# Kernel optimization log

Measured on AMD Instinct MI355X. Metric: run time of the kernel, lower is better.

Reference implementation:

```python
import jax, jax.numpy as jnp
import numpy as np

D_MODEL = 1024
N_HEADS = 16
HEAD_DIM = D_MODEL // N_HEADS  # 64
WINDOW = 128
LOCAL_BLOCK = 256
LATENT_TOKENS = 64
LATENT_D = 256
LATENT_HEADS = 4
LATENT_HD = LATENT_D // LATENT_HEADS  # 64
NEG = -1e9


def setup_inputs() -> dict:
    key = jax.random.key(0)
    ks = jax.random.split(key, 14)
    B, S = 2, 4096
    s = 0.02
    f32 = jnp.float32
    return {
        "x": jax.random.normal(ks[0], (B, S, D_MODEL), f32),
        "qkv_w": jax.random.normal(ks[1], (D_MODEL, 3 * D_MODEL), f32) * s,
        "qkv_b": jnp.zeros((3 * D_MODEL,), f32),
        "rq_w": jax.random.normal(ks[2], (D_MODEL, LATENT_D), f32) * s,
        "rq_b": jnp.zeros((LATENT_D,), f32),
        "rkv_w": jax.random.normal(ks[3], (D_MODEL, 2 * LATENT_D), f32) * s,
        "rkv_b": jnp.zeros((2 * LATENT_D,), f32),
        "rout_w": jax.random.normal(ks[4], (LATENT_D, D_MODEL), f32) * s,
        "rout_b": jnp.zeros((D_MODEL,), f32),
        "out_w": jax.random.normal(ks[5], (D_MODEL, D_MODEL), f32) * s,
        "out_b": jnp.zeros((D_MODEL,), f32),
        "gl_w": jax.random.normal(ks[6], (HEAD_DIM, 1), f32) * s,
        "gr_w": jax.random.normal(ks[7], (HEAD_DIM, 1), f32) * s,
    }


def _local_attention(q, k, v):
    # q,k,v: [B,H,S,hd]. Blockwise causal local attention: query i attends to
    # keys at distance d with 0 < d <= WINDOW (strictly past, self excluded).
    B, H, S, hd = q.shape
    bs = min(S, max(WINDOW, LOCAL_BLOCK))
    nb = S // bs  # S chosen divisible by bs
    w = WINDOW
    L = bs + w - 1  # key span per query block
    k_pad = jnp.pad(k, ((0, 0), (0, 0), (w - 1, 0), (0, 0)))
    v_pad = jnp.pad(v, ((0, 0), (0, 0), (w - 1, 0), (0, 0)))
    starts = jnp.arange(nb) * bs
    idx = starts[:, None] + jnp.arange(L)[None, :]  # [nb,L] into padded axis
    kb = k_pad[:, :, idx]  # [B,H,nb,L,hd]
    vb = v_pad[:, :, idx]
    qb = q.reshape(B, H, nb, bs, hd)
    q_pos = starts[:, None] + jnp.arange(bs)[None, :]            # [nb,bs]
    k_gpos = starts[:, None] + jnp.arange(L)[None, :] - (w - 1)   # [nb,L]
    dist = q_pos[:, :, None] - k_gpos[:, None, :]                 # [nb,bs,L]
    allowed = (dist > 0) & (dist <= w) & (k_gpos[:, None, :] >= 0)
    scale = 1.0 / np.sqrt(hd)
    scores = jnp.einsum('bhnqd,bhnkd->bhnqk', qb, kb) * scale
    scores = jnp.where(allowed, scores, NEG)
    attn = jax.nn.softmax(scores, axis=-1)
    # query 0 has no valid keys (self excluded) -> output 0 for that row
    attn = jnp.where(allowed.any(-1)[None, None, :, :, None], attn, 0.0)
    out = jnp.einsum('bhnqk,bhnkd->bhnqd', attn, vb)
    return out.reshape(B, H, S, hd)


def reference(x, qkv_w, qkv_b, rq_w, rq_b, rkv_w, rkv_b, rout_w, rout_b,
              out_w, out_b, gl_w, gr_w):
    B, S, D = x.shape
    # ---- local branch ----
    qkv = x @ qkv_w + qkv_b  # [B,S,3D]
    q, k, v = jnp.split(qkv, 3, axis=-1)
    def heads(t):
        return t.reshape(B, S, N_HEADS, HEAD_DIM).transpose(0, 2, 1, 3)
    local = _local_attention(heads(q), heads(k), heads(v))  # [B,H,S,hd]
    # ---- pooled latents ----
    chunk = -(-S // min(LATENT_TOKENS, S))  # ceil; S divisible here
    nlat = S // chunk
    pooled = x.reshape(B, nlat, chunk, D).mean(axis=2)  # [B,L,D]
    chunk_ids = jnp.arange(S) // chunk                   # [S]
    # ---- latent cross-attention ----
    rq = (x @ rq_w + rq_b).reshape(B, S, LATENT_HEADS, LATENT_HD).transpose(0, 2, 1, 3)
    rkv = pooled @ rkv_w + rkv_b
    rk, rv = jnp.split(rkv, 2, axis=-1)
    rk = rk.reshape(B, nlat, LATENT_HEADS, LATENT_HD).transpose(0, 2, 1, 3)
    rv = rv.reshape(B, nlat, LATENT_HEADS, LATENT_HD).transpose(0, 2, 1, 3)
    lscale = 1.0 / np.sqrt(LATENT_HD)
    lscores = jnp.einsum('bhsd,bhld->bhsl', rq, rk) * lscale  # [B,Hl,S,L]
    lat_allowed = jnp.arange(nlat)[None, :] < chunk_ids[:, None]  # strictly past chunks
    lscores = jnp.where(lat_allowed[None, None], lscores, NEG)
    lattn = jax.nn.softmax(lscores, axis=-1)
    lattn = jnp.where(lat_allowed.any(-1)[None, None, :, None], lattn, 0.0)
    lat_out = jnp.einsum('bhsl,bhld->bhsd', lattn, rv)  # [B,Hl,S,hdl]
    lat_out = lat_out.transpose(0, 2, 1, 3).reshape(B, S, LATENT_D)
    remote = (lat_out @ rout_w + rout_b)                 # [B,S,D]
    remote_h = remote.reshape(B, S, N_HEADS, HEAD_DIM).transpose(0, 2, 1, 3)
    # ---- learned per-head gate mixing local/remote ----
    gate = jax.nn.sigmoid(local @ gl_w + remote_h @ gr_w)  # [B,H,S,1]
    mixed = gate * local + (1.0 - gate) * remote_h
    mixed = mixed.transpose(0, 2, 1, 3).reshape(B, S, D)
    return mixed @ out_w + out_b
```

## Files before the change

### kernel.cpp

```cpp
#include <hip/hip_runtime.h>

typedef __bf16 bf16;
typedef bf16 bf16x4 __attribute__((ext_vector_type(4)));
typedef bf16 bf16x8 __attribute__((ext_vector_type(8)));
typedef float f32x4 __attribute__((ext_vector_type(4)));

#define B_ 2
#define S_ 4096
#define D_ 1024
#define QSTR 3328

__device__ __forceinline__ void gload_lds16(const void* g, void* l) {
  __builtin_amdgcn_global_load_lds((const __attribute__((address_space(1))) void*)g,
                                   (__attribute__((address_space(3))) void*)l, 16, 0, 0);
}

__device__ __forceinline__ void transpose_block(
    const float* __restrict__ in, bf16* __restrict__ out, int K, int N,
    int bx, int by, float (*tile)[33], int tx, int ty)
{
  const int nb = bx * 32, kb = by * 32;
#pragma unroll
  for (int j = 0; j < 4; j++)
    tile[ty + j * 8][tx] = in[(size_t)(kb + ty + j * 8) * N + nb + tx];
  __syncthreads();
#pragma unroll
  for (int j = 0; j < 4; j++)
    out[(size_t)(nb + ty + j * 8) * K + kb + tx] = (bf16)tile[tx][ty + j * 8];
}

__global__ __launch_bounds__(256) void prep_kernel(
    const float* __restrict__ qkv_w, const float* __restrict__ rq_w,
    const float* __restrict__ rkv_w, const float* __restrict__ rout_w,
    const float* __restrict__ out_w, const float* __restrict__ x,
    const float* __restrict__ qkv_b, const float* __restrict__ rq_b,
    bf16* __restrict__ qkvr_wt, bf16* __restrict__ rkv_wt,
    bf16* __restrict__ rout_wt, bf16* __restrict__ out_wt,
    bf16* __restrict__ xb, float* __restrict__ qkvr_b)
{
  __shared__ float tile[32][33];
  const int t = threadIdx.x;
  const int tx = t & 31, ty = t >> 5;
  int bid = blockIdx.x;
  if (bid < 3072) {
    transpose_block(qkv_w, qkvr_wt, 1024, 3072, bid % 96, bid / 96, tile, tx, ty);
    return;
  }
  bid -= 3072;
  if (bid < 256) {
    transpose_block(rq_w, qkvr_wt + (size_t)3072 * 1024, 1024, 256, bid % 8, bid / 8, tile, tx, ty);
    return;
  }
  bid -= 256;
  if (bid < 512) {
    transpose_block(rkv_w, rkv_wt, 1024, 512, bid % 16, bid / 16, tile, tx, ty);
    return;
  }
  bid -= 512;
  if (bid < 256) {
    transpose_block(rout_w, rout_wt, 256, 1024, bid % 32, bid / 32, tile, tx, ty);
    return;
  }
  bid -= 256;
  if (bid < 1024) {
    transpose_block(out_w, out_wt, 1024, 1024, bid % 32, bid / 32, tile, tx, ty);
    return;
  }
  bid -= 1024;
  if (bid < 2048) {
    const int n4 = B_ * S_ * 1024 / 4;
    for (int i = bid * 256 + t; i < n4; i += 2048 * 256) {
      const float4 v = ((const float4*)x)[i];
      bf16x4 o = {(bf16)v.x, (bf16)v.y, (bf16)v.z, (bf16)v.w};
      *(bf16x4*)&xb[i * 4] = o;
    }
    return;
  }
  {
    for (int i = t; i < 3072; i += 256) qkvr_b[i] = qkv_b[i];
    if (t < 256) qkvr_b[3072 + t] = rq_b[t];
  }
}

template <typename OutT>
__global__ __launch_bounds__(256) void gemm_bias_kernel(
    const bf16* __restrict__ A, const bf16* __restrict__ Bt,
    const float* __restrict__ bias, OutT* __restrict__ C,
    int M, int N, int K)
{
  __shared__ __align__(16) bf16 Al[128 * 32];
  __shared__ __align__(16) bf16 Bl[128 * 32];
  const int m0 = blockIdx.x * 128;
  const int n0 = blockIdx.y * 128;
  const int t = threadIdx.x;
  const int lane = t & 63;
  const int wave = t >> 6;
  const int wr = (wave >> 1) * 64;
  const int wc = (wave & 1) * 64;
  const int r16 = lane & 15;
  const int kg = lane >> 4;

  f32x4 acc[4][4];
#pragma unroll
  for (int i = 0; i < 4; i++)
#pragma unroll
    for (int j = 0; j < 4; j++) {
      f32x4 z = {0.f, 0.f, 0.f, 0.f};
      acc[i][j] = z;
    }

  for (int k0 = 0; k0 < K; k0 += 32) {
    __syncthreads();
#pragma unroll
    for (int i = 0; i < 2; i++) {
      const int o = i * 4096 + wave * 1024 + lane * 16;
      const int r = o >> 6;
      const int cb = o & 63;
      gload_lds16((const char*)(A + (size_t)(m0 + r) * K + k0) + cb,
                  (char*)Al + i * 4096 + wave * 1024);
      gload_lds16((const char*)(Bt + (size_t)(n0 + r) * K + k0) + cb,
                  (char*)Bl + i * 4096 + wave * 1024);
    }
    __syncthreads();
    bf16x8 a[4], b[4];
#pragma unroll
    for (int i = 0; i < 4; i++)
      a[i] = *(const bf16x8*)&Al[(wr + i * 16 + r16) * 32 + kg * 8];
#pragma unroll
    for (int i = 0; i < 4; i++)
      b[i] = *(const bf16x8*)&Bl[(wc + i * 16 + r16) * 32 + kg * 8];
#pragma unroll
    for (int i = 0; i < 4; i++)
#pragma unroll
      for (int j = 0; j < 4; j++)
        acc[i][j] = __builtin_amdgcn_mfma_f32_16x16x32_bf16(a[i], b[j], acc[i][j], 0, 0, 0);
  }

  float bs[4];
#pragma unroll
  for (int j = 0; j < 4; j++) bs[j] = bias[n0 + wc + j * 16 + r16];
#pragma unroll
  for (int i = 0; i < 4; i++)
#pragma unroll
    for (int j = 0; j < 4; j++)
#pragma unroll
      for (int r = 0; r < 4; r++) {
        const int row = m0 + wr + i * 16 + kg * 4 + r;
        const int col = n0 + wc + j * 16 + r16;
        C[(size_t)row * N + col] = (OutT)(acc[i][j][r] + bs[j]);
      }
}

template <typename OutT>
__global__ __launch_bounds__(512, 1) void gemm8_kernel(
    const bf16* __restrict__ A, const bf16* __restrict__ Bt,
    const float* __restrict__ bias, OutT* __restrict__ C,
    int M, int N, int K)
{
  __shared__ __align__(16) bf16 Al[2][256 * 64];
  __shared__ __align__(16) bf16 Bl[2][256 * 64];

  const int nbx = gridDim.x;
  const int nwg = nbx * gridDim.y;
  int bid = blockIdx.y * nbx + blockIdx.x;
  bid = (bid & 7) * (nwg >> 3) + (bid >> 3);
  const int m0 = (bid % nbx) * 256;
  const int n0 = (bid / nbx) * 256;

  const int t = threadIdx.x;
  const int lane = t & 63;
  const int w = t >> 6;
  const int wm = w >> 2;
  const int wn = w & 3;
  const int l15 = lane & 15;
  const int kg = lane >> 4;

  const int srow = t >> 3;
  const int schunk = (t & 7) ^ (srow & 7);
  const bf16* Aaddr = A + (size_t)(m0 + srow) * K + schunk * 8;
  const bf16* Baddr = Bt + (size_t)(n0 + srow) * K + schunk * 8;

  const int NT = K >> 6;
  const int NITER = NT >> 1;

  const int arow = wm * 128 + l15;
  const int brow = wn * 64 + l15;
  const int c0 = (kg ^ (l15 & 7)) * 16;
  const int c1 = ((4 + kg) ^ (l15 & 7)) * 16;

  f32x4 acc[8][4];
#pragma unroll
  for (int i = 0; i < 8; i++)
#pragma unroll
    for (int j = 0; j < 4; j++) { f32x4 z = {0, 0, 0, 0}; acc[i][j] = z; }

#define STG_A(buf, q, kt) gload_lds16(Aaddr + (size_t)(q) * 64 * K + (kt) * 64, \
                                      (char*)&Al[buf][0] + (q) * 8192 + w * 1024)
#define STG_B(buf, q, kt) gload_lds16(Baddr + (size_t)(q) * 64 * K + (kt) * 64, \
                                      (char*)&Bl[buf][0] + (q) * 8192 + w * 1024)
#define RD_A(buf, aq) \
  _Pragma("unroll") for (int ii = 0; ii < 4; ii++) { \
    const char* p_ = (const char*)&Al[buf][0] + (size_t)(arow + (aq) * 64 + ii * 16) * 128; \
    af[ii][0] = *(const bf16x8*)(p_ + c0); \
    af[ii][1] = *(const bf16x8*)(p_ + c1); }
#define RD_B(buf) \
  _Pragma("unroll") for (int jj = 0; jj < 4; jj++) { \
    const char* p_ = (const char*)&Bl[buf][0] + (size_t)(brow + jj * 16) * 128; \
    bfr[jj][0] = *(const bf16x8*)(p_ + c0); \
    bfr[jj][1] = *(const bf16x8*)(p_ + c1); }
#define MM(iofs, j0) \
  _Pragma("unroll") for (int ii = 0; ii < 4; ii++) \
  _Pragma("unroll") for (int jj = (j0); jj < (j0) + 2; jj++) { \
    acc[(iofs) + ii][jj] = __builtin_amdgcn_mfma_f32_16x16x32_bf16(af[ii][0], bfr[jj][0], acc[(iofs) + ii][jj], 0, 0, 0); \
    acc[(iofs) + ii][jj] = __builtin_amdgcn_mfma_f32_16x16x32_bf16(af[ii][1], bfr[jj][1], acc[(iofs) + ii][jj], 0, 0, 0); }
#define BARX __builtin_amdgcn_s_barrier()
#define LGKMD asm volatile("s_waitcnt lgkmcnt(0)" ::: "memory")
#define PRI1 __builtin_amdgcn_s_setprio(1)
#define PRI0 __builtin_amdgcn_s_setprio(0)

#pragma unroll
  for (int q = 0; q < 4; q++) { STG_B(0, q, 0); }
#pragma unroll
  for (int q = 0; q < 4; q++) { STG_A(0, q, 0); }
#pragma unroll
  for (int q = 0; q < 4; q++) { STG_B(1, q, 1); }
#pragma unroll
  for (int q = 0; q < 4; q++) { STG_A(1, q, 1); }
  asm volatile("s_waitcnt vmcnt(8)" ::: "memory");
  BARX;

  bf16x8 af[4][2], bfr[4][2];

  for (int it = 0; it < NITER; it++) {
    const int kt0 = 2 * it;
    const bool st = (it + 1) < NITER;

    RD_A(0, 0); RD_B(0);
    PRI1; MM(0, 0); PRI0; LGKMD; BARX;
    if (st) { STG_B(0, 0, kt0 + 2); STG_B(0, 1, kt0 + 2); }
    PRI1; MM(0, 2); PRI0; BARX;
    RD_A(0, 1);
    if (st) { STG_B(0, 2, kt0 + 2); STG_B(0, 3, kt0 + 2); }
    PRI1; MM(4, 0); PRI0; LGKMD; BARX;
    if (st) { STG_A(0, 0, kt0 + 2); STG_A(0, 2, kt0 + 2); }
    PRI1; MM(4, 2); PRI0;
    asm volatile("s_waitcnt vmcnt(6)" ::: "memory");
    BARX;

    RD_A(1, 0); RD_B(1);
    if (st) { STG_A(0, 1, kt0 + 2); STG_A(0, 3, kt0 + 2); }
    PRI1; MM(0, 0); PRI0; LGKMD; BARX;
    if (st) { STG_B(1, 0, kt0 + 3); STG_B(1, 1, kt0 + 3); }
    PRI1; MM(0, 2); PRI0; BARX;
    RD_A(1, 1);
    if (st) { STG_B(1, 2, kt0 + 3); STG_B(1, 3, kt0 + 3); }
    PRI1; MM(4, 0); PRI0; LGKMD; BARX;
    if (st) { STG_A(1, 0, kt0 + 3); STG_A(1, 1, kt0 + 3);
              STG_A(1, 2, kt0 + 3); STG_A(1, 3, kt0 + 3); }
    PRI1; MM(4, 2); PRI0;
    asm volatile("s_waitcnt vmcnt(8)" ::: "memory");
    BARX;
  }

#undef STG_A
#undef STG_B
#undef RD_A
#undef RD_B
#undef MM
#undef BARX
#undef LGKMD
#undef PRI1
#undef PRI0

  float bs[4];
#pragma unroll
  for (int j = 0; j < 4; j++) bs[j] = bias[n0 + wn * 64 + j * 16 + l15];
#pragma unroll
  for (int i = 0; i < 8; i++)
#pragma unroll
    for (int j = 0; j < 4; j++)
#pragma unroll
      for (int rr = 0; rr < 4; rr++) {
        const int row = m0 + wm * 128 + i * 16 + kg * 4 + rr;
        const int col = n0 + wn * 64 + j * 16 + l15;
        C[(size_t)row * N + col] = (OutT)(acc[i][j][rr] + bs[j]);
      }
}

__global__ __launch_bounds__(256) void pool_rkv_kernel(
    const bf16* __restrict__ xb, const bf16* __restrict__ rkv_wt,
    const float* __restrict__ rkv_b, bf16* __restrict__ rkvb)
{
  __shared__ float prow[1024];
  const int blk = blockIdx.x;
  const int b = blk >> 6, lt = blk & 63;
  const int t = threadIdx.x;

  const bf16* px = xb + ((size_t)b * S_ + lt * 64) * 1024 + t * 4;
  float s0 = 0.f, s1 = 0.f, s2 = 0.f, s3 = 0.f;
#pragma unroll
  for (int c = 0; c < 64; c++) {
    bf16x4 v = *(const bf16x4*)(px + (size_t)c * 1024);
    s0 += (float)v[0]; s1 += (float)v[1]; s2 += (float)v[2]; s3 += (float)v[3];
  }
  prow[t * 4 + 0] = s0 * 0.015625f;
  prow[t * 4 + 1] = s1 * 0.015625f;
  prow[t * 4 + 2] = s2 * 0.015625f;
  prow[t * 4 + 3] = s3 * 0.015625f;
  __syncthreads();

  const int n = blockIdx.y * 256 + t;
  const bf16* wcol = rkv_wt + (size_t)n * 1024;
  float s = rkv_b[n];
#pragma unroll 4
  for (int k = 0; k < 1024; k += 8) {
    bf16x8 wv = *(const bf16x8*)(wcol + k);
#pragma unroll
    for (int j = 0; j < 8; j++) s += prow[k + j] * (float)wv[j];
  }
  rkvb[(size_t)blk * 512 + n] = (bf16)s;
}

__global__ __launch_bounds__(256) void latent_attn_kernel(
    const bf16* __restrict__ qkvrb, const bf16* __restrict__ rkvb,
    bf16* __restrict__ latout)
{
  __shared__ float rq_s[256];
  __shared__ float attn_s[4][64];
  const int blk = blockIdx.x;
  const int b = blk >> 12, s = blk & 4095;
  const int t = threadIdx.x;
  const int h = t >> 6, l = t & 63;
  const int cid = s >> 6;
  rq_s[t] = (float)qkvrb[((size_t)b * S_ + s) * QSTR + 3072 + t];
  __syncthreads();
  float val = -1e30f;
  if (l < cid) {
    const bf16* kr = rkvb + (size_t)(b * 64 + l) * 512 + h * 64;
    float sum = 0.f;
#pragma unroll
    for (int c = 0; c < 8; c++) {
      bf16x8 kv = *(const bf16x8*)(kr + c * 8);
#pragma unroll
      for (int j = 0; j < 8; j++) sum += rq_s[h * 64 + c * 8 + j] * (float)kv[j];
    }
    val = sum * 0.125f;
  }
  float mx = val;
#pragma unroll
  for (int off = 32; off; off >>= 1) mx = fmaxf(mx, __shfl_xor(mx, off));
  const float p = (l < cid) ? __expf(val - mx) : 0.f;
  float sm = p;
#pragma unroll
  for (int off = 32; off; off >>= 1) sm += __shfl_xor(sm, off);
  attn_s[h][l] = (sm > 0.f) ? p / sm : 0.f;
  __syncthreads();
  float o = 0.f;
  const bf16* vb = rkvb + (size_t)b * 64 * 512 + 256 + h * 64 + l;
  for (int lat = 0; lat < cid; lat++) o += attn_s[h][lat] * (float)vb[(size_t)lat * 512];
  latout[((size_t)b * S_ + s) * 256 + h * 64 + l] = (bf16)o;
}

__global__ __launch_bounds__(256, 4) void local_attn_gate(
    const bf16* __restrict__ qkv, const bf16* __restrict__ remote,
    const float* __restrict__ glw, const float* __restrict__ grw,
    bf16* __restrict__ mixedb)
{
  __shared__ __align__(16) bf16 Kl[128 * 72];
  __shared__ __align__(16) bf16 Vt[64 * 136];
  __shared__ __align__(16) bf16 Pl[4][16 * 136];

  const int q0 = blockIdx.x * 128;
  const int h  = blockIdx.y;
  const int b  = blockIdx.z;
  const int t  = threadIdx.x;
  const int w  = t >> 6;
  const int l  = t & 63;
  const int g  = l >> 4;
  const int l15 = l & 15;

  const bf16* qbase = qkv + (size_t)b * S_ * QSTR + h * 64;
  const bf16* kbase = qbase + 1024;
  const bf16* vbase = qbase + 2048;

  bf16* PlW = &Pl[w][0];

  const int vrow = (t >> 3) * 4;
  const int vdh  = (t & 7) * 8;

  bf16x8 qf[2][2];
#pragma unroll
  for (int sl = 0; sl < 2; sl++) {
    const int j = sl ? 7 - w : w;
#pragma unroll
    for (int db = 0; db < 2; db++)
      qf[sl][db] = *(const bf16x8*)(qbase + (size_t)(q0 + j * 16 + l15) * QSTR + db * 32 + g * 8);
  }

  float m_[2][4], l_[2][4];
  f32x4 accO[2][4];
#pragma unroll
  for (int sl = 0; sl < 2; sl++) {
#pragma unroll
    for (int r = 0; r < 4; r++) { m_[sl][r] = -1e30f; l_[sl][r] = 0.f; }
#pragma unroll
    for (int dt = 0; dt < 4; dt++) { f32x4 z = {0,0,0,0}; accO[sl][dt] = z; }
  }

  const int tstart = (q0 == 0) ? 1 : 0;

  for (int tile = tstart; tile < 2; tile++) {
    const int base = q0 - 128 + tile * 128;
    bf16x8 kreg[4], vreg[4];
#pragma unroll
    for (int i = 0; i < 4; i++) {
      const int c = i * 256 + t;
      const int kk = c >> 3, dc = c & 7;
      kreg[i] = *(const bf16x8*)(kbase + (size_t)(base + kk) * QSTR + dc * 8);
    }
#pragma unroll
    for (int i = 0; i < 4; i++)
      vreg[i] = *(const bf16x8*)(vbase + (size_t)(base + vrow + i) * QSTR + vdh);

    __syncthreads();
#pragma unroll
    for (int i = 0; i < 4; i++) {
      const int c = i * 256 + t;
      const int kk = c >> 3, dc = c & 7;
      *(bf16x8*)&Kl[kk * 72 + dc * 8] = kreg[i];
    }
#pragma unroll
    for (int j = 0; j < 8; j++) {
      bf16x4 wv = {vreg[0][j], vreg[1][j], vreg[2][j], vreg[3][j]};
      *(bf16x4*)&Vt[(vdh + j) * 136 + vrow] = wv;
    }
    __syncthreads();

#pragma unroll
    for (int sl = 0; sl < 2; sl++) {
      const int j = sl ? 7 - w : w;
      const int lo = (tile == 0) ? (j & ~1) : 0;
      const int hi = (tile == 0) ? 8 : ((j & ~1) + 2);

      f32x4 s[8];
      __builtin_amdgcn_s_setprio(1);
#pragma unroll
      for (int kk = 0; kk < 8; kk++) {
        if (kk < lo || kk >= hi) continue;
        f32x4 z = {0,0,0,0};
        s[kk] = z;
        const bf16x8 kf0 = *(const bf16x8*)&Kl[(kk * 16 + l15) * 72 + g * 8];
        const bf16x8 kf1 = *(const bf16x8*)&Kl[(kk * 16 + l15) * 72 + 32 + g * 8];
        s[kk] = __builtin_amdgcn_mfma_f32_16x16x32_bf16(qf[sl][0], kf0, s[kk], 0, 0, 0);
        s[kk] = __builtin_amdgcn_mfma_f32_16x16x32_bf16(qf[sl][1], kf1, s[kk], 0, 0, 0);
      }
      __builtin_amdgcn_s_setprio(0);
#pragma unroll
      for (int kk = 0; kk < 8; kk++) {
        if (kk < lo || kk >= hi) continue;
        const int kr = kk * 16 + l15;
#pragma unroll
        for (int r = 0; r < 4; r++) {
          const int qr = j * 16 + g * 4 + r;
          const bool ok = (tile == 0) ? (kr >= qr) : (kr < qr);
          s[kk][r] = ok ? s[kk][r] * 0.125f : -1e9f;
        }
      }
      float corr[4];
#pragma unroll
      for (int r = 0; r < 4; r++) {
        float v = -1e30f;
#pragma unroll
        for (int kk = 0; kk < 8; kk++) { if (kk < lo || kk >= hi) continue; v = fmaxf(v, s[kk][r]); }
        v = fmaxf(v, __shfl_xor(v, 1));
        v = fmaxf(v, __shfl_xor(v, 2));
        v = fmaxf(v, __shfl_xor(v, 4));
        v = fmaxf(v, __shfl_xor(v, 8));
        const float mn = fmaxf(m_[sl][r], v);
        corr[r] = __expf(m_[sl][r] - mn);
        m_[sl][r] = mn;
      }
      float rs[4] = {0.f, 0.f, 0.f, 0.f};
#pragma unroll
      for (int kk = 0; kk < 8; kk++) {
        if (kk < lo || kk >= hi) continue;
#pragma unroll
        for (int r = 0; r < 4; r++) {
          const float sv = s[kk][r];
          const float p = (sv > -5e8f) ? __expf(sv - m_[sl][r]) : 0.f;
          rs[r] += p;
          PlW[(g * 4 + r) * 136 + kk * 16 + l15] = (bf16)p;
        }
      }
#pragma unroll
      for (int r = 0; r < 4; r++) {
        float v = rs[r];
        v += __shfl_xor(v, 1); v += __shfl_xor(v, 2);
        v += __shfl_xor(v, 4); v += __shfl_xor(v, 8);
        l_[sl][r] = l_[sl][r] * corr[r] + v;
#pragma unroll
        for (int dt = 0; dt < 4; dt++) accO[sl][dt][r] *= corr[r];
      }
      const int clo = (tile == 0) ? (j >> 1) : 0;
      const int chi = (tile == 0) ? 4 : ((j >> 1) + 1);
      __builtin_amdgcn_s_setprio(1);
#pragma unroll
      for (int kc = 0; kc < 4; kc++) {
        if (kc < clo || kc >= chi) continue;
        const bf16x8 pa = *(const bf16x8*)&PlW[l15 * 136 + kc * 32 + g * 8];
#pragma unroll
        for (int dt = 0; dt < 4; dt++) {
          const bf16x8 vf = *(const bf16x8*)&Vt[(dt * 16 + l15) * 136 + kc * 32 + g * 8];
          accO[sl][dt] = __builtin_amdgcn_mfma_f32_16x16x32_bf16(pa, vf, accO[sl][dt], 0, 0, 0);
        }
      }
      __builtin_amdgcn_s_setprio(0);
    }
  }

  float glv[4], grv[4];
#pragma unroll
  for (int dt = 0; dt < 4; dt++) {
    glv[dt] = glw[dt * 16 + l15];
    grv[dt] = grw[dt * 16 + l15];
  }
  bf16* outp = mixedb + ((size_t)b * S_ + q0) * 1024 + h * 64;
  const bf16* rbase = remote + ((size_t)b * S_ + q0) * 1024 + h * 64;
#pragma unroll
  for (int sl = 0; sl < 2; sl++) {
    const int j = sl ? 7 - w : w;
#pragma unroll
    for (int r = 0; r < 4; r++) {
      const int row = j * 16 + g * 4 + r;
      const float inv = (l_[sl][r] > 0.f) ? 1.f / l_[sl][r] : 0.f;
      float lv[4], rv[4];
      float part = 0.f;
#pragma unroll
      for (int dt = 0; dt < 4; dt++) {
        lv[dt] = accO[sl][dt][r] * inv;
        rv[dt] = (float)rbase[(size_t)row * 1024 + dt * 16 + l15];
        part += lv[dt] * glv[dt] + rv[dt] * grv[dt];
      }
      part += __shfl_xor(part, 1);
      part += __shfl_xor(part, 2);
      part += __shfl_xor(part, 4);
      part += __shfl_xor(part, 8);
      const float gg = 1.f / (1.f + __expf(-part));
#pragma unroll
      for (int dt = 0; dt < 4; dt++)
        outp[(size_t)row * 1024 + dt * 16 + l15] = (bf16)(gg * lv[dt] + (1.f - gg) * rv[dt]);
    }
  }
}

extern "C" void kernel_launch(void* const* d_in, const int* in_sizes, int n_in,
                              void* d_out, int out_size, void* d_ws, size_t ws_size,
                              hipStream_t stream)
{
  const float* x      = (const float*)d_in[0];
  const float* qkv_w  = (const float*)d_in[1];
  const float* qkv_b  = (const float*)d_in[2];
  const float* rq_w   = (const float*)d_in[3];
  const float* rq_b   = (const float*)d_in[4];
  const float* rkv_w  = (const float*)d_in[5];
  const float* rkv_b  = (const float*)d_in[6];
  const float* rout_w = (const float*)d_in[7];
  const float* rout_b = (const float*)d_in[8];
  const float* out_w  = (const float*)d_in[9];
  const float* out_b  = (const float*)d_in[10];
  const float* gl_w   = (const float*)d_in[11];
  const float* gr_w   = (const float*)d_in[12];

  char* w = (char*)d_ws;
  bf16* qkvr_wt = (bf16*)w; w += (size_t)QSTR * 1024 * 2;
  bf16* rkv_wt  = (bf16*)w; w += (size_t)512 * 1024 * 2;
  bf16* rout_wt = (bf16*)w; w += (size_t)1024 * 256 * 2;
  bf16* out_wt  = (bf16*)w; w += (size_t)1024 * 1024 * 2;
  float* qkvr_b = (float*)w; w += (size_t)QSTR * 4;
  bf16* xb      = (bf16*)w; w += (size_t)B_ * S_ * 1024 * 2;
  bf16* qkvrb   = (bf16*)w; w += (size_t)B_ * S_ * QSTR * 2;
  bf16* rkvb    = (bf16*)w; w += (size_t)B_ * 64 * 512 * 2;
  bf16* latout  = (bf16*)w; w += (size_t)B_ * S_ * 256 * 2;
  bf16* remote  = (bf16*)w; w += (size_t)B_ * S_ * 1024 * 2;
  bf16* mixedb  = (bf16*)w; w += (size_t)B_ * S_ * 1024 * 2;

  prep_kernel<<<dim3(7169), 256, 0, stream>>>(qkv_w, rq_w, rkv_w, rout_w, out_w, x,
                                              qkv_b, rq_b,
                                              qkvr_wt, rkv_wt, rout_wt, out_wt, xb, qkvr_b);

  gemm8_kernel<bf16><<<dim3(32, 13), 512, 0, stream>>>(xb, qkvr_wt, qkvr_b, qkvrb, B_ * S_, QSTR, 1024);
  pool_rkv_kernel<<<dim3(128, 2), 256, 0, stream>>>(xb, rkv_wt, rkv_b, rkvb);
  latent_attn_kernel<<<dim3(B_ * S_), 256, 0, stream>>>(qkvrb, rkvb, latout);
  gemm_bias_kernel<bf16><<<dim3(64, 8), 256, 0, stream>>>(latout, rout_wt, rout_b, remote, B_ * S_, 1024, 256);
  local_attn_gate<<<dim3(S_ / 128, 16, B_), 256, 0, stream>>>(qkvrb, remote, gl_w, gr_w, mixedb);
  gemm_bias_kernel<float><<<dim3(64, 8), 256, 0, stream>>>(mixedb, out_wt, out_b, (float*)d_out, B_ * S_, 1024, 1024);
}
```

Before: 216.0 us.

## Restructure GEMM mainloop into per-tile pipeline with staggered A/B prefetch

Replaces the two-tile unrolled mainloop with a single-k-tile loop that alternates LDS buffers. A is prefetched one tile ahead into the other buffer, and B is prefetched two tiles ahead into the buffer being consumed, once its reads are done. B fragment reads are split into two halves, so MFMA phases interleave more finely with LDS reads and global-to-LDS loads. The intent is better overlap of memory traffic with MFMA work. The cost is more barriers per tile and careful vmcnt and lgkmcnt accounting, which could create hazards or stalls.

```diff
diff --git a/kernel.cpp b/kernel.cpp
--- a/kernel.cpp
+++ b/kernel.cpp
@@ -181,7 +181,6 @@
   const bf16* Baddr = Bt + (size_t)(n0 + srow) * K + schunk * 8;
 
   const int NT = K >> 6;
-  const int NITER = NT >> 1;
 
   const int arow = wm * 128 + l15;
   const int brow = wn * 64 + l15;
@@ -194,17 +193,28 @@
 #pragma unroll
     for (int j = 0; j < 4; j++) { f32x4 z = {0, 0, 0, 0}; acc[i][j] = z; }
 
-#define STG_A(buf, q, kt) gload_lds16(Aaddr + (size_t)(q) * 64 * K + (kt) * 64, \
-                                      (char*)&Al[buf][0] + (q) * 8192 + w * 1024)
-#define STG_B(buf, q, kt) gload_lds16(Baddr + (size_t)(q) * 64 * K + (kt) * 64, \
-                                      (char*)&Bl[buf][0] + (q) * 8192 + w * 1024)
+#define STG_A(buf, half, kt) do { \
+  gload_lds16(Aaddr + (size_t)((half) * 128) * K + (kt) * 64, \
+              (char*)&Al[buf][0] + (half) * 16384 + w * 1024); \
+  gload_lds16(Aaddr + (size_t)((half) * 128 + 64) * K + (kt) * 64, \
+              (char*)&Al[buf][0] + (half) * 16384 + 8192 + w * 1024); } while (0)
+#define STG_B(buf, half, kt) do { \
+  gload_lds16(Baddr + (size_t)((half) * 128) * K + (kt) * 64, \
+              (char*)&Bl[buf][0] + (half) * 16384 + w * 1024); \
+  gload_lds16(Baddr + (size_t)((half) * 128 + 64) * K + (kt) * 64, \
+              (char*)&Bl[buf][0] + (half) * 16384 + 8192 + w * 1024); } while (0)
 #define RD_A(buf, aq) \
   _Pragma("unroll") for (int ii = 0; ii < 4; ii++) { \
     const char* p_ = (const char*)&Al[buf][0] + (size_t)(arow + (aq) * 64 + ii * 16) * 128; \
     af[ii][0] = *(const bf16x8*)(p_ + c0); \
     af[ii][1] = *(const bf16x8*)(p_ + c1); }
-#define RD_B(buf) \
-  _Pragma("unroll") for (int jj = 0; jj < 4; jj++) { \
+#define RD_B01(buf) \
+  _Pragma("unroll") for (int jj = 0; jj < 2; jj++) { \
+    const char* p_ = (const char*)&Bl[buf][0] + (size_t)(brow + jj * 16) * 128; \
+    bfr[jj][0] = *(const bf16x8*)(p_ + c0); \
+    bfr[jj][1] = *(const bf16x8*)(p_ + c1); }
+#define RD_B23(buf) \
+  _Pragma("unroll") for (int jj = 2; jj < 4; jj++) { \
     const char* p_ = (const char*)&Bl[buf][0] + (size_t)(brow + jj * 16) * 128; \
     bfr[jj][0] = *(const bf16x8*)(p_ + c0); \
     bfr[jj][1] = *(const bf16x8*)(p_ + c1); }
@@ -214,61 +224,54 @@
     acc[(iofs) + ii][jj] = __builtin_amdgcn_mfma_f32_16x16x32_bf16(af[ii][0], bfr[jj][0], acc[(iofs) + ii][jj], 0, 0, 0); \
     acc[(iofs) + ii][jj] = __builtin_amdgcn_mfma_f32_16x16x32_bf16(af[ii][1], bfr[jj][1], acc[(iofs) + ii][jj], 0, 0, 0); }
 #define BARX __builtin_amdgcn_s_barrier()
-#define LGKMD asm volatile("s_waitcnt lgkmcnt(0)" ::: "memory")
+#define LGKM0 asm volatile("s_waitcnt lgkmcnt(0)" ::: "memory")
 #define PRI1 __builtin_amdgcn_s_setprio(1)
 #define PRI0 __builtin_amdgcn_s_setprio(0)
 
-#pragma unroll
-  for (int q = 0; q < 4; q++) { STG_B(0, q, 0); }
-#pragma unroll
-  for (int q = 0; q < 4; q++) { STG_A(0, q, 0); }
-#pragma unroll
-  for (int q = 0; q < 4; q++) { STG_B(1, q, 1); }
-#pragma unroll
-  for (int q = 0; q < 4; q++) { STG_A(1, q, 1); }
-  asm volatile("s_waitcnt vmcnt(8)" ::: "memory");
+  STG_B(0, 0, 0); STG_B(0, 1, 0);
+  STG_A(0, 0, 0); STG_A(0, 1, 0);
+  if (1 < NT) { STG_B(1, 0, 1); STG_B(1, 1, 1); }
+  asm volatile("s_waitcnt vmcnt(4)" ::: "memory");
   BARX;
 
   bf16x8 af[4][2], bfr[4][2];
 
-  for (int it = 0; it < NITER; it++) {
-    const int kt0 = 2 * it;
-    const bool st = (it + 1) < NITER;
-
-    RD_A(0, 0); RD_B(0);
-    PRI1; MM(0, 0); PRI0; LGKMD; BARX;
-    if (st) { STG_B(0, 0, kt0 + 2); STG_B(0, 1, kt0 + 2); }
+  for (int kt = 0; kt < NT; kt++) {
+    const int cur = kt & 1;
+    const int nxt = cur ^ 1;
+    const bool stA = (kt + 1) < NT;
+    const bool stB = (kt + 2) < NT;
+
+    RD_A(cur, 0); RD_B01(cur);
+    if (stA) STG_A(nxt, 0, kt + 1);
+    asm volatile("s_waitcnt lgkmcnt(8)" ::: "memory");
+    BARX; LGKM0;
+    PRI1; MM(0, 0); PRI0; BARX;
+
+    RD_B23(cur);
+    if (stA) STG_A(nxt, 1, kt + 1);
+    BARX; LGKM0;
     PRI1; MM(0, 2); PRI0; BARX;
-    RD_A(0, 1);
-    if (st) { STG_B(0, 2, kt0 + 2); STG_B(0, 3, kt0 + 2); }
-    PRI1; MM(4, 0); PRI0; LGKMD; BARX;
-    if (st) { STG_A(0, 0, kt0 + 2); STG_A(0, 2, kt0 + 2); }
+
+    RD_A(cur, 1);
+    if (stB) STG_B(cur, 0, kt + 2);
+    BARX; LGKM0;
+    PRI1; MM(4, 0); PRI0; BARX;
+
+    if (stB) STG_B(cur, 1, kt + 2);
     PRI1; MM(4, 2); PRI0;
-    asm volatile("s_waitcnt vmcnt(6)" ::: "memory");
-    BARX;
-
-    RD_A(1, 0); RD_B(1);
-    if (st) { STG_A(0, 1, kt0 + 2); STG_A(0, 3, kt0 + 2); }
-    PRI1; MM(0, 0); PRI0; LGKMD; BARX;
-    if (st) { STG_B(1, 0, kt0 + 3); STG_B(1, 1, kt0 + 3); }
-    PRI1; MM(0, 2); PRI0; BARX;
-    RD_A(1, 1);
-    if (st) { STG_B(1, 2, kt0 + 3); STG_B(1, 3, kt0 + 3); }
-    PRI1; MM(4, 0); PRI0; LGKMD; BARX;
-    if (st) { STG_A(1, 0, kt0 + 3); STG_A(1, 1, kt0 + 3);
-              STG_A(1, 2, kt0 + 3); STG_A(1, 3, kt0 + 3); }
-    PRI1; MM(4, 2); PRI0;
-    asm volatile("s_waitcnt vmcnt(8)" ::: "memory");
+    asm volatile("s_waitcnt vmcnt(4)" ::: "memory");
     BARX;
   }
 
 #undef STG_A
 #undef STG_B
 #undef RD_A
-#undef RD_B
+#undef RD_B01
+#undef RD_B23
 #undef MM
 #undef BARX
-#undef LGKMD
+#undef LGKM0
 #undef PRI1
 #undef PRI0
 
```

After: 219.7 us. About the same (+1.7%).
